# Performance work log

Hardware: AMD Instinct MI355X
Metric: run time of the kernel (lower is better)

## Reference

```python
import jax, jax.numpy as jnp
import numpy as np

B, S, D, H, F = 2, 4096, 768, 12, 3072
DK = D // H
EPS = 1e-5


def _layernorm(x, alpha, gamma):
    # Faithful to the custom Layernormalization: torch.std (unbiased, ddof=1),
    # (x - mean) / (std + eps), scalar alpha/gamma.
    m = jnp.mean(x, axis=-1, keepdims=True)
    s = jnp.std(x, axis=-1, ddof=1, keepdims=True)
    return alpha * ((x - m) / (s + EPS)) + gamma


def setup_inputs() -> dict:
    key = jax.random.key(0)
    ks = jax.random.split(key, 12)
    sc = 0.02
    inp = {
        "x": jax.random.normal(ks[0], (B, S, D), jnp.float32),
        # attention projections, stored as [in, out]
        "wq": jax.random.normal(ks[1], (D, D), jnp.float32) * sc,
        "bq": jnp.zeros((D,), jnp.float32),
        "wk": jax.random.normal(ks[2], (D, D), jnp.float32) * sc,
        "bk": jnp.zeros((D,), jnp.float32),
        "wv": jax.random.normal(ks[3], (D, D), jnp.float32) * sc,
        "bv": jnp.zeros((D,), jnp.float32),
        "wo": jax.random.normal(ks[4], (D, D), jnp.float32) * sc,
        "bo": jnp.zeros((D,), jnp.float32),
        # feedforward
        "w1": jax.random.normal(ks[5], (D, F), jnp.float32) * sc,
        "b1": jnp.zeros((F,), jnp.float32),
        "w2": jax.random.normal(ks[6], (F, D), jnp.float32) * sc,
        "b2": jnp.zeros((D,), jnp.float32),
        # two residual LayerNorms, scalar params (alpha=1, gamma=0 at init)
        "a1": jnp.ones((1,), jnp.float32),
        "g1": jnp.zeros((1,), jnp.float32),
        "a2": jnp.ones((1,), jnp.float32),
        "g2": jnp.zeros((1,), jnp.float32),
    }
    return inp


def reference(x, wq, bq, wk, bk, wv, bv, wo, bo, w1, b1, w2, b2, a1, g1, a2, g2):
    # --- self attention sublayer ---
    q = (x @ wq + bq).reshape(B, S, H, DK).transpose(0, 2, 1, 3)  # [B,H,S,dk]
    k = (x @ wk + bk).reshape(B, S, H, DK).transpose(0, 2, 1, 3)
    v = (x @ wv + bv).reshape(B, S, H, DK).transpose(0, 2, 1, 3)
    scores = jnp.einsum("bhqd,bhkd->bhqk", q, k) / np.sqrt(DK).astype(np.float32)
    attn = jax.nn.softmax(scores, axis=-1)  # dropout is identity (p=0 / eval)
    ctx = jnp.einsum("bhqk,bhkd->bhqd", attn, v)  # [B,H,S,dk]
    ctx = ctx.transpose(0, 2, 1, 3).reshape(B, S, D)
    attn_out = ctx @ wo + bo
    x = _layernorm(x + attn_out, a1, g1)
    # --- feedforward sublayer ---
    ff = jax.nn.relu(x @ w1 + b1) @ w2 + b2
    x = _layernorm(x + ff, a2, g2)
    return x
```

## Files before the change

### kernel.cpp

```cpp
#include <hip/hip_runtime.h>
#include <hip/hip_bf16.h>
#include <cstdint>
#include <cstddef>

typedef unsigned short u16;
typedef __attribute__((ext_vector_type(8))) __bf16 bf16x8;
typedef __attribute__((ext_vector_type(4))) float f32x4;

#define AS1 __attribute__((address_space(1)))
#define AS3 __attribute__((address_space(3)))

__device__ __forceinline__ u16 f2bf(float f) {
    union { float f; uint32_t u; } v; v.f = f;
    uint32_t r = (v.u + 0x7FFFu + ((v.u >> 16) & 1u)) >> 16;
    return (u16)r;
}

__device__ __forceinline__ float bf2f(u16 b) {
    union { uint32_t u; float f; } v; v.u = ((uint32_t)b) << 16;
    return v.f;
}

__device__ __forceinline__ uint32_t pack_bf2(float lo, float hi) {
    __hip_bfloat162 p = __float22bfloat162_rn(float2{lo, hi});
    union { __hip_bfloat162 b; uint32_t u; } v; v.b = p;
    return v.u;
}

__device__ __forceinline__ f32x4 mfma16(bf16x8 a, bf16x8 b, f32x4 c) {
    return __builtin_amdgcn_mfma_f32_16x16x32_bf16(a, b, c, 0, 0, 0);
}

__device__ __forceinline__ void async16(const u16* g, u16* lds_uniform_base) {
    __builtin_amdgcn_global_load_lds((const AS1 void*)g, (AS3 void*)lds_uniform_base, 16, 0, 0);
}

__device__ __forceinline__ int xcd_swz(int nwg) {
    int b = blockIdx.x + gridDim.x * (blockIdx.y + gridDim.y * blockIdx.z);
    return (b & 7) * (nwg >> 3) + (b >> 3);
}

__global__ __launch_bounds__(256)
void k_prep(const float* __restrict__ x, u16* __restrict__ xb,
            const float* __restrict__ wq, const float* __restrict__ wk,
            const float* __restrict__ wv, const float* __restrict__ wo,
            const float* __restrict__ w1, const float* __restrict__ w2,
            u16* __restrict__ wqkvt, u16* __restrict__ wot,
            u16* __restrict__ w1t, u16* __restrict__ w2t)
{
    int bx = blockIdx.x;
    if (bx < 6144) {
        int i = (bx * 256 + threadIdx.x) * 4;
        float4 f = *(const float4*)(x + i);
        xb[i + 0] = f2bf(f.x); xb[i + 1] = f2bf(f.y);
        xb[i + 2] = f2bf(f.z); xb[i + 3] = f2bf(f.w);
        return;
    }
    int t = bx - 6144;
    const float* in; u16* out; int R, C;
    if (t < 2304) {
        int m = t / 576; t -= m * 576;
        R = 768; C = 768;
        in = (m == 0) ? wq : (m == 1) ? wk : (m == 2) ? wv : wo;
        out = (m < 3) ? wqkvt + (size_t)m * 768 * 768 : wot;
    } else if (t < 4608) {
        t -= 2304; in = w1; out = w1t; R = 768; C = 3072;
    } else {
        t -= 4608; in = w2; out = w2t; R = 3072; C = 768;
    }
    int tilesX = C >> 5;
    int c0 = (t % tilesX) * 32, r0 = (t / tilesX) * 32;
    __shared__ float tile[32][33];
    int tx = threadIdx.x & 31, ty = threadIdx.x >> 5;
    #pragma unroll
    for (int i = ty; i < 32; i += 8)
        tile[i][tx] = in[(size_t)(r0 + i) * C + c0 + tx];
    __syncthreads();
    #pragma unroll
    for (int i = ty; i < 32; i += 8)
        out[(size_t)(c0 + i) * R + r0 + tx] = f2bf(tile[tx][i]);
}

template <bool RELU>
__global__ __launch_bounds__(256)
void k_gemm(const u16* __restrict__ A, const u16* __restrict__ Bt,
            const float* __restrict__ bias, u16* __restrict__ Cb,
            int M, int N, int K)
{
    __shared__ __align__(16) u16 lA[2 * 4096];
    __shared__ __align__(16) u16 lB[2 * 4096];
    const int tid = threadIdx.x;
    const int w = tid >> 6, lane = tid & 63;
    const int quad = lane >> 4, l15 = lane & 15;
    const int m0 = blockIdx.x * 128, n0 = blockIdx.y * 128;
    const int wm = (w >> 1) * 64, wn = (w & 1) * 64;
    const int sw = (quad ^ ((l15 >> 1) & 3)) * 8;
    const int dst = (w * 64) * 8;

    const u16* pA[2]; const u16* pB[2];
    #pragma unroll
    for (int r = 0; r < 2; ++r) {
        int c = r * 256 + tid;
        int row = c >> 2, ch = (c & 3) ^ ((row >> 1) & 3);
        pA[r] = A + (size_t)(m0 + row) * K + ch * 8;
        pB[r] = Bt + (size_t)(n0 + row) * K + ch * 8;
    }

    const f32x4 fz = {0.f, 0.f, 0.f, 0.f};
    f32x4 acc[4][4];
    #pragma unroll
    for (int i = 0; i < 4; ++i)
        #pragma unroll
        for (int j = 0; j < 4; ++j) acc[i][j] = fz;

    #pragma unroll
    for (int r = 0; r < 2; ++r) {
        async16(pA[r], lA + r * 2048 + dst);
        async16(pB[r], lB + r * 2048 + dst);
        pA[r] += 32; pB[r] += 32;
    }

    const int nIt = K >> 5;
    for (int it = 0; it < nIt; ++it) {
        __syncthreads();
        if (it + 1 < nIt) {
            int nb = (it + 1) & 1;
            #pragma unroll
            for (int r = 0; r < 2; ++r) {
                async16(pA[r], lA + nb * 4096 + r * 2048 + dst);
                async16(pB[r], lB + nb * 4096 + r * 2048 + dst);
                pA[r] += 32; pB[r] += 32;
            }
        }
        const u16* bA = lA + (it & 1) * 4096;
        const u16* bB = lB + (it & 1) * 4096;
        bf16x8 af[4], bfr[4];
        #pragma unroll
        for (int i = 0; i < 4; ++i)
            af[i] = *(const bf16x8*)&bA[(wm + i * 16 + l15) * 32 + sw];
        #pragma unroll
        for (int j = 0; j < 4; ++j)
            bfr[j] = *(const bf16x8*)&bB[(wn + j * 16 + l15) * 32 + sw];
        #pragma unroll
        for (int i = 0; i < 4; ++i)
            #pragma unroll
            for (int j = 0; j < 4; ++j)
                acc[i][j] = mfma16(af[i], bfr[j], acc[i][j]);
    }
    #pragma unroll
    for (int j = 0; j < 4; ++j) {
        int col = n0 + wn + j * 16 + l15;
        float bv = bias[col];
        #pragma unroll
        for (int i = 0; i < 4; ++i) {
            int row = m0 + wm + i * 16 + quad * 4;
            #pragma unroll
            for (int r = 0; r < 4; ++r) {
                float t = acc[i][j][r] + bv;
                if (RELU) t = fmaxf(t, 0.f);
                Cb[(size_t)(row + r) * N + col] = f2bf(t);
            }
        }
    }
}

__global__ __launch_bounds__(256)
void k_gemm_part(const u16* __restrict__ A, const u16* __restrict__ Bt,
                 float* __restrict__ C0, float* __restrict__ C1,
                 int M, int N, int K, int Kh)
{
    __shared__ __align__(16) u16 lA[2 * 4096];
    __shared__ __align__(16) u16 lB[2 * 4096];
    const int tid = threadIdx.x;
    const int w = tid >> 6, lane = tid & 63;
    const int quad = lane >> 4, l15 = lane & 15;
    const int m0 = blockIdx.x * 128, n0 = blockIdx.y * 128;
    const int wm = (w >> 1) * 64, wn = (w & 1) * 64;
    const int sw = (quad ^ ((l15 >> 1) & 3)) * 8;
    const int kbeg = blockIdx.z * Kh;
    float* __restrict__ C = blockIdx.z ? C1 : C0;
    const int dst = (w * 64) * 8;

    const u16* pA[2]; const u16* pB[2];
    #pragma unroll
    for (int r = 0; r < 2; ++r) {
        int c = r * 256 + tid;
        int row = c >> 2, ch = (c & 3) ^ ((row >> 1) & 3);
        pA[r] = A + (size_t)(m0 + row) * K + kbeg + ch * 8;
        pB[r] = Bt + (size_t)(n0 + row) * K + kbeg + ch * 8;
    }

    const f32x4 fz = {0.f, 0.f, 0.f, 0.f};
    f32x4 acc[4][4];
    #pragma unroll
    for (int i = 0; i < 4; ++i)
        #pragma unroll
        for (int j = 0; j < 4; ++j) acc[i][j] = fz;

    #pragma unroll
    for (int r = 0; r < 2; ++r) {
        async16(pA[r], lA + r * 2048 + dst);
        async16(pB[r], lB + r * 2048 + dst);
        pA[r] += 32; pB[r] += 32;
    }

    const int nIt = Kh >> 5;
    for (int it = 0; it < nIt; ++it) {
        __syncthreads();
        if (it + 1 < nIt) {
            int nb = (it + 1) & 1;
            #pragma unroll
            for (int r = 0; r < 2; ++r) {
                async16(pA[r], lA + nb * 4096 + r * 2048 + dst);
                async16(pB[r], lB + nb * 4096 + r * 2048 + dst);
                pA[r] += 32; pB[r] += 32;
            }
        }
        const u16* bA = lA + (it & 1) * 4096;
        const u16* bB = lB + (it & 1) * 4096;
        bf16x8 af[4], bfr[4];
        #pragma unroll
        for (int i = 0; i < 4; ++i)
            af[i] = *(const bf16x8*)&bA[(wm + i * 16 + l15) * 32 + sw];
        #pragma unroll
        for (int j = 0; j < 4; ++j)
            bfr[j] = *(const bf16x8*)&bB[(wn + j * 16 + l15) * 32 + sw];
        #pragma unroll
        for (int i = 0; i < 4; ++i)
            #pragma unroll
            for (int j = 0; j < 4; ++j)
                acc[i][j] = mfma16(af[i], bfr[j], acc[i][j]);
    }
    #pragma unroll
    for (int j = 0; j < 4; ++j) {
        int col = n0 + wn + j * 16 + l15;
        #pragma unroll
        for (int i = 0; i < 4; ++i) {
            int row = m0 + wm + i * 16 + quad * 4;
            #pragma unroll
            for (int r = 0; r < 4; ++r)
                C[(size_t)(row + r) * N + col] = acc[i][j][r];
        }
    }
}

__global__ __launch_bounds__(256)
void k_gemm_qkv(const u16* __restrict__ A, const u16* __restrict__ Bt,
                const float* __restrict__ bq, const float* __restrict__ bk,
                const float* __restrict__ bv,
                u16* __restrict__ qb, u16* __restrict__ kb, u16* __restrict__ vtg,
                int M, int K, float scale_q)
{
    __shared__ __align__(16) u16 qsm[4 * 64 * 72];
    u16* lA = qsm;
    u16* lB = qsm + 8192;
    const int tid = threadIdx.x;
    const int w = tid >> 6, lane = tid & 63;
    const int quad = lane >> 4, l15 = lane & 15;
    const int m0 = blockIdx.x * 128, n0 = blockIdx.y * 128;
    const int wm = (w >> 1) * 64, wn = (w & 1) * 64;
    const int sw = (quad ^ ((l15 >> 1) & 3)) * 8;
    const int sel = blockIdx.y / 6;
    const int cl0 = n0 - sel * 768;
    const int dst = (w * 64) * 8;

    const u16* pA[2]; const u16* pB[2];
    #pragma unroll
    for (int r = 0; r < 2; ++r) {
        int c = r * 256 + tid;
        int row = c >> 2, ch = (c & 3) ^ ((row >> 1) & 3);
        pA[r] = A + (size_t)(m0 + row) * K + ch * 8;
        pB[r] = Bt + (size_t)(n0 + row) * K + ch * 8;
    }

    const f32x4 fz = {0.f, 0.f, 0.f, 0.f};
    f32x4 acc[4][4];
    #pragma unroll
    for (int i = 0; i < 4; ++i)
        #pragma unroll
        for (int j = 0; j < 4; ++j) acc[i][j] = fz;

    #pragma unroll
    for (int r = 0; r < 2; ++r) {
        async16(pA[r], lA + r * 2048 + dst);
        async16(pB[r], lB + r * 2048 + dst);
        pA[r] += 32; pB[r] += 32;
    }

    const int nIt = K >> 5;
    for (int it = 0; it < nIt; ++it) {
        __syncthreads();
        if (it + 1 < nIt) {
            int nb = (it + 1) & 1;
            #pragma unroll
            for (int r = 0; r < 2; ++r) {
                async16(pA[r], lA + nb * 4096 + r * 2048 + dst);
                async16(pB[r], lB + nb * 4096 + r * 2048 + dst);
                pA[r] += 32; pB[r] += 32;
            }
        }
        const u16* bA = lA + (it & 1) * 4096;
        const u16* bB = lB + (it & 1) * 4096;
        bf16x8 af[4], bfr[4];
        #pragma unroll
        for (int i = 0; i < 4; ++i)
            af[i] = *(const bf16x8*)&bA[(wm + i * 16 + l15) * 32 + sw];
        #pragma unroll
        for (int j = 0; j < 4; ++j)
            bfr[j] = *(const bf16x8*)&bB[(wn + j * 16 + l15) * 32 + sw];
        #pragma unroll
        for (int i = 0; i < 4; ++i)
            #pragma unroll
            for (int j = 0; j < 4; ++j)
                acc[i][j] = mfma16(af[i], bfr[j], acc[i][j]);
    }
    __syncthreads();
    const float* bias = (sel == 0) ? bq : (sel == 1) ? bk : bv;
    if (sel < 2) {
        u16* out = (sel == 0) ? qb : kb;
        float sc = (sel == 0) ? scale_q : 1.f;
        #pragma unroll
        for (int j = 0; j < 4; ++j) {
            int cl = cl0 + wn + j * 16 + l15;
            float bvv = bias[cl];
            #pragma unroll
            for (int i = 0; i < 4; ++i) {
                int row = m0 + wm + i * 16 + quad * 4;
                #pragma unroll
                for (int r = 0; r < 4; ++r)
                    out[(size_t)(row + r) * 768 + cl] = f2bf((acc[i][j][r] + bvv) * sc);
            }
        }
    } else {
        u16* lT = qsm + w * 4608;
        #pragma unroll
        for (int j = 0; j < 4; ++j) {
            float bvv = bias[cl0 + wn + j * 16 + l15];
            #pragma unroll
            for (int i = 0; i < 4; ++i)
                #pragma unroll
                for (int r = 0; r < 4; ++r)
                    lT[(j * 16 + l15) * 72 + i * 16 + quad * 4 + r]
                        = f2bf(acc[i][j][r] + bvv);
        }
        int gcol = cl0 + wn + lane;
        u16* gdst = vtg + (size_t)gcol * M + m0 + wm;
        #pragma unroll
        for (int kk = 0; kk < 8; ++kk) {
            bf16x8 v = *(const bf16x8*)&lT[lane * 72 + kk * 8];
            *(bf16x8*)(gdst + kk * 8) = v;
        }
    }
}

__global__ __launch_bounds__(256, 3)
void k_attention(const u16* __restrict__ Q, const u16* __restrict__ Kb,
                 const u16* __restrict__ Vt, u16* __restrict__ ctx,
                 int S, int D, int H, int M)
{
    __shared__ __align__(16) u16 sKV[16384];
    __shared__ float sL[2][64];
    const int o = xcd_swz(gridDim.x * gridDim.y);
    const int qt = o % gridDim.x, bh = o / gridDim.x;
    const int b = bh / H, h = bh % H;
    const int tid = threadIdx.x, w = tid >> 6, lane = tid & 63;
    const int wq = w & 1, wk = w >> 1;
    const int quad = lane >> 4, l15 = lane & 15;
    const int sw = (quad ^ ((l15 >> 1) & 3)) * 8;
    const size_t bS = (size_t)b * S;
    const int q0 = qt * 128 + wq * 64;

    bf16x8 qf[4][2];
    #pragma unroll
    for (int set = 0; set < 4; ++set)
        #pragma unroll
        for (int kc = 0; kc < 2; ++kc)
            qf[set][kc] = *(const bf16x8*)(Q + (bS + q0 + set * 16 + l15) * D
                                           + (size_t)h * 64 + kc * 32 + quad * 8);

    const f32x4 fz = {0.f, 0.f, 0.f, 0.f};
    f32x4 O[4][4], Ol[4];
    #pragma unroll
    for (int s = 0; s < 4; ++s) {
        Ol[s] = fz;
        #pragma unroll
        for (int j = 0; j < 4; ++j) O[s][j] = fz;
    }
    union { u16 s[8]; bf16x8 v; } one8;
    #pragma unroll
    for (int i = 0; i < 8; ++i) one8.s[i] = 0x3F80;

    const u16* kbase = Kb + bS * D + (size_t)h * 64;
    const u16* vbase = Vt + (size_t)h * 64 * M + bS;

    const int rsw = (lane & ~12) | ((lane & 4) << 1) | ((lane & 8) >> 1);
    const u16* gk[2]; const u16* gv[2];
    #pragma unroll
    for (int i = 0; i < 2; ++i) {
        gk[i] = kbase + (size_t)rsw * D + i * 32 + w * 8;
        int c = i * 256 + tid;
        int dk = (c >> 2) & 63, vch = (c & 3) ^ ((dk >> 1) & 3);
        gv[i] = vbase + (size_t)dk * M + i * 32 + vch * 8;
    }
    const int dslot = w * 512;

    #pragma unroll
    for (int i = 0; i < 2; ++i) {
        async16(gk[i], sKV + i * 2048 + dslot);
        async16(gv[i], sKV + 8192 + i * 2048 + dslot);
        gk[i] += (size_t)64 * D;
        gv[i] += 64;
    }

    int ksl[2];
    #pragma unroll
    for (int ks = 0; ks < 2; ++ks) {
        int row64 = wk * 32 + ((l15 >> 2) << 3) + ks * 4 + (l15 & 3);
        int s = (row64 & ~12) | ((row64 & 4) << 1) | ((row64 & 8) >> 1);
        ksl[ks] = quad * 512 + s * 8;
    }

    const int T = S >> 6;
    for (int t = 0; t < T; ++t) {
        __syncthreads();
        if (t + 1 < T) {
            int nb = (t + 1) & 1;
            #pragma unroll
            for (int i = 0; i < 2; ++i) {
                async16(gk[i], sKV + nb * 4096 + i * 2048 + dslot);
                async16(gv[i], sKV + 8192 + nb * 4096 + i * 2048 + dslot);
                gk[i] += (size_t)64 * D;
                gv[i] += 64;
            }
        }
        const u16* lKb = sKV + (t & 1) * 4096;
        const u16* lVb = sKV + 8192 + (t & 1) * 4096;

        bf16x8 ka[2][2], vf[4];
        #pragma unroll
        for (int ks = 0; ks < 2; ++ks)
            #pragma unroll
            for (int kc = 0; kc < 2; ++kc)
                ka[ks][kc] = *(const bf16x8*)&lKb[kc * 2048 + ksl[ks]];
        #pragma unroll
        for (int dj = 0; dj < 4; ++dj)
            vf[dj] = *(const bf16x8*)
                &lVb[wk * 2048 + (dj * 16 + l15) * 32 + sw];

        #pragma unroll
        for (int set = 0; set < 4; ++set) {
            f32x4 sc0 = fz, sc1 = fz;
            __builtin_amdgcn_s_setprio(1);
            sc0 = mfma16(ka[0][0], qf[set][0], sc0);
            sc0 = mfma16(ka[0][1], qf[set][1], sc0);
            sc1 = mfma16(ka[1][0], qf[set][0], sc1);
            sc1 = mfma16(ka[1][1], qf[set][1], sc1);
            __builtin_amdgcn_s_setprio(0);
            float p0[4], p1[4];
            #pragma unroll
            for (int r = 0; r < 4; ++r) {
                p0[r] = __builtin_amdgcn_exp2f(sc0[r]);
                p1[r] = __builtin_amdgcn_exp2f(sc1[r]);
            }
            union { uint32_t u[4]; bf16x8 v; } pa;
            pa.u[0] = pack_bf2(p0[0], p0[1]); pa.u[1] = pack_bf2(p0[2], p0[3]);
            pa.u[2] = pack_bf2(p1[0], p1[1]); pa.u[3] = pack_bf2(p1[2], p1[3]);
            __builtin_amdgcn_s_setprio(1);
            #pragma unroll
            for (int dj = 0; dj < 4; ++dj)
                O[set][dj] = mfma16(pa.v, vf[dj], O[set][dj]);
            Ol[set] = mfma16(pa.v, one8.v, Ol[set]);
            __builtin_amdgcn_s_setprio(0);
        }
    }

    __syncthreads();
    u16* lO = sKV;
    if (wk == 1) {
        #pragma unroll
        for (int set = 0; set < 4; ++set) {
            #pragma unroll
            for (int dj = 0; dj < 4; ++dj)
                #pragma unroll
                for (int r = 0; r < 4; ++r)
                    lO[(wq * 64 + set * 16 + quad * 4 + r) * 66 + dj * 16 + l15]
                        = f2bf(O[set][dj][r]);
            if (l15 == 0) {
                #pragma unroll
                for (int r = 0; r < 4; ++r)
                    sL[wq][set * 16 + quad * 4 + r] = Ol[set][r];
            }
        }
    }
    __syncthreads();
    if (wk == 0) {
        #pragma unroll
        for (int set = 0; set < 4; ++set) {
            float rl[4];
            #pragma unroll
            for (int r = 0; r < 4; ++r)
                rl[r] = 1.f / (Ol[set][r] + sL[wq][set * 16 + quad * 4 + r]);
            #pragma unroll
            for (int dj = 0; dj < 4; ++dj)
                #pragma unroll
                for (int r = 0; r < 4; ++r) {
                    float o = O[set][dj][r]
                        + bf2f(lO[(wq * 64 + set * 16 + quad * 4 + r) * 66 + dj * 16 + l15]);
                    ctx[(bS + q0 + set * 16 + quad * 4 + r) * D
                        + (size_t)h * 64 + dj * 16 + l15] = f2bf(o * rl[r]);
                }
        }
    }
}

__global__ __launch_bounds__(256)
void k_layernorm2(const float* __restrict__ p0, const float* __restrict__ p1,
                  const float* __restrict__ resid, const float* __restrict__ bias,
                  const float* __restrict__ a, const float* __restrict__ g,
                  float* __restrict__ outf, u16* __restrict__ outb, int D)
{
    const int row = blockIdx.x, tid = threadIdx.x;
    const size_t base = (size_t)row * D;
    float v[3];
    float s = 0.f, sq = 0.f;
    #pragma unroll
    for (int i = 0; i < 3; ++i) {
        int c = tid + i * 256;
        float x = p0[base + c] + p1[base + c] + resid[base + c] + bias[c];
        v[i] = x; s += x; sq += x * x;
    }
    #pragma unroll
    for (int off = 32; off >= 1; off >>= 1) {
        s += __shfl_xor(s, off, 64);
        sq += __shfl_xor(sq, off, 64);
    }
    __shared__ float red[8];
    const int w = tid >> 6;
    if ((tid & 63) == 0) { red[w] = s; red[4 + w] = sq; }
    __syncthreads();
    s = red[0] + red[1] + red[2] + red[3];
    sq = red[4] + red[5] + red[6] + red[7];
    float mean = s / D;
    float var = fmaxf((sq - s * mean) / (D - 1), 0.f);
    float denom = sqrtf(var) + 1e-5f;
    float av = a[0], gv = g[0];
    #pragma unroll
    for (int i = 0; i < 3; ++i) {
        float y = av * ((v[i] - mean) / denom) + gv;
        if (outf) outf[base + tid + i * 256] = y;
        if (outb) outb[base + tid + i * 256] = f2bf(y);
    }
}

extern "C" void kernel_launch(void* const* d_in, const int* in_sizes, int n_in,
                              void* d_out, int out_size, void* d_ws, size_t ws_size,
                              hipStream_t stream)
{
    constexpr int B = 2, S = 4096, D = 768, H = 12, F = 3072;
    constexpr int M = B * S;
    const float SCALE_Q = 1.4426950408889634f / 8.0f;
    const float* x  = (const float*)d_in[0];
    const float* wq = (const float*)d_in[1];
    const float* bq = (const float*)d_in[2];
    const float* wk = (const float*)d_in[3];
    const float* bk = (const float*)d_in[4];
    const float* wv = (const float*)d_in[5];
    const float* bv = (const float*)d_in[6];
    const float* wo = (const float*)d_in[7];
    const float* bo = (const float*)d_in[8];
    const float* w1 = (const float*)d_in[9];
    const float* b1 = (const float*)d_in[10];
    const float* w2 = (const float*)d_in[11];
    const float* b2 = (const float*)d_in[12];
    const float* a1 = (const float*)d_in[13];
    const float* g1 = (const float*)d_in[14];
    const float* a2 = (const float*)d_in[15];
    const float* g2 = (const float*)d_in[16];

    char* ws = (char*)d_ws;
    size_t off = 0;
    auto alloc = [&](size_t bytes) {
        void* p = ws + off;
        off = (off + bytes + 255) & ~(size_t)255;
        return p;
    };
    u16*   xb    = (u16*)alloc((size_t)M * D * 2);
    u16*   wqkvt = (u16*)alloc((size_t)3 * D * D * 2);
    u16*   wot   = (u16*)alloc((size_t)D * D * 2);
    u16*   w1t   = (u16*)alloc((size_t)D * F * 2);
    u16*   w2t   = (u16*)alloc((size_t)D * F * 2);
    u16*   qb    = (u16*)alloc((size_t)M * D * 2);
    u16*   kb    = (u16*)alloc((size_t)M * D * 2);
    u16*   vtg   = (u16*)alloc((size_t)M * D * 2);
    u16*   ctxb  = (u16*)alloc((size_t)M * D * 2);
    float* x1f   = (float*)alloc((size_t)M * D * 4);
    u16*   x1b   = (u16*)alloc((size_t)M * D * 2);
    u16*   ff1b  = (u16*)alloc((size_t)M * F * 2);

    float* p0a = (float*)qb;
    float* p1a = (float*)ff1b;
    float* p0b = (float*)qb;
    float* p1b = (float*)vtg;

    k_prep<<<6144 + 6912, 256, 0, stream>>>(x, xb, wq, wk, wv, wo, w1, w2,
                                            wqkvt, wot, w1t, w2t);

    k_gemm_qkv<<<dim3(M / 128, 3 * D / 128), 256, 0, stream>>>(
        xb, wqkvt, bq, bk, bv, qb, kb, vtg, M, D, SCALE_Q);

    k_attention<<<dim3(S / 128, B * H), 256, 0, stream>>>(qb, kb, vtg, ctxb, S, D, H, M);

    k_gemm_part<<<dim3(M / 128, D / 128, 2), 256, 0, stream>>>(
        ctxb, wot, p0a, p1a, M, D, D, D / 2);
    k_layernorm2<<<M, 256, 0, stream>>>(p0a, p1a, x, bo, a1, g1, x1f, x1b, D);

    k_gemm<true><<<dim3(M / 128, F / 128), 256, 0, stream>>>(
        x1b, w1t, b1, ff1b, M, F, D);
    k_gemm_part<<<dim3(M / 128, D / 128, 2), 256, 0, stream>>>(
        ff1b, w2t, p0b, p1b, M, D, F, F / 2);
    k_layernorm2<<<M, 256, 0, stream>>>(p0b, p1b, x1f, b2, a2, g2, (float*)d_out, nullptr, D);

    (void)in_sizes; (void)n_in; (void)out_size; (void)ws_size;
}
```

Baseline: 451.7 us.

## Triple-buffer GEMM LDS tiles with prefetch distance two and explicit vmcnt waits

Converts the three GEMM kernels (generic, split-K partial, QKV) from double-buffered to triple-buffered LDS staging. Two K-tiles are issued ahead and each iteration waits only for the oldest group via s_waitcnt vmcnt(4) before a raw s_barrier, instead of a full __syncthreads drain. The goal is to keep more global loads in flight so memory latency hides behind the MFMA work. In exchange LDS use per block grows from 32 KB to 48 KB, which may lower occupancy, and correctness now depends on the exact count of outstanding async loads per thread.

```diff
diff --git a/kernel.cpp b/kernel.cpp
--- a/kernel.cpp
+++ b/kernel.cpp
@@ -87,15 +87,15 @@
             const float* __restrict__ bias, u16* __restrict__ Cb,
             int M, int N, int K)
 {
-    __shared__ __align__(16) u16 lA[2 * 4096];
-    __shared__ __align__(16) u16 lB[2 * 4096];
+    __shared__ __align__(16) u16 lA[3 * 4096];
+    __shared__ __align__(16) u16 lB[3 * 4096];
     const int tid = threadIdx.x;
     const int w = tid >> 6, lane = tid & 63;
     const int quad = lane >> 4, l15 = lane & 15;
     const int m0 = blockIdx.x * 128, n0 = blockIdx.y * 128;
     const int wm = (w >> 1) * 64, wn = (w & 1) * 64;
     const int sw = (quad ^ ((l15 >> 1) & 3)) * 8;
-    const int dst = (w * 64) * 8;
+    const int dst = w * 512;
 
     const u16* pA[2]; const u16* pB[2];
     #pragma unroll
@@ -114,17 +114,24 @@
         for (int j = 0; j < 4; ++j) acc[i][j] = fz;
 
     #pragma unroll
-    for (int r = 0; r < 2; ++r) {
-        async16(pA[r], lA + r * 2048 + dst);
-        async16(pB[r], lB + r * 2048 + dst);
-        pA[r] += 32; pB[r] += 32;
+    for (int p = 0; p < 2; ++p) {
+        #pragma unroll
+        for (int r = 0; r < 2; ++r) {
+            async16(pA[r], lA + p * 4096 + r * 2048 + dst);
+            async16(pB[r], lB + p * 4096 + r * 2048 + dst);
+            pA[r] += 32; pB[r] += 32;
+        }
     }
 
     const int nIt = K >> 5;
+    int cur = 0;
     for (int it = 0; it < nIt; ++it) {
-        __syncthreads();
-        if (it + 1 < nIt) {
-            int nb = (it + 1) & 1;
+        if (it + 1 < nIt) asm volatile("s_waitcnt vmcnt(4)" ::: "memory");
+        else              asm volatile("s_waitcnt vmcnt(0)" ::: "memory");
+        __builtin_amdgcn_s_barrier();
+        asm volatile("" ::: "memory");
+        if (it + 2 < nIt) {
+            int nb = cur + 2; if (nb >= 3) nb -= 3;
             #pragma unroll
             for (int r = 0; r < 2; ++r) {
                 async16(pA[r], lA + nb * 4096 + r * 2048 + dst);
@@ -132,8 +139,8 @@
                 pA[r] += 32; pB[r] += 32;
             }
         }
-        const u16* bA = lA + (it & 1) * 4096;
-        const u16* bB = lB + (it & 1) * 4096;
+        const u16* bA = lA + cur * 4096;
+        const u16* bB = lB + cur * 4096;
         bf16x8 af[4], bfr[4];
         #pragma unroll
         for (int i = 0; i < 4; ++i)
@@ -146,6 +153,8 @@
             #pragma unroll
             for (int j = 0; j < 4; ++j)
                 acc[i][j] = mfma16(af[i], bfr[j], acc[i][j]);
+        asm volatile("" ::: "memory");
+        cur = (cur + 1 == 3) ? 0 : cur + 1;
     }
     #pragma unroll
     for (int j = 0; j < 4; ++j) {
@@ -169,8 +178,8 @@
                  float* __restrict__ C0, float* __restrict__ C1,
                  int M, int N, int K, int Kh)
 {
-    __shared__ __align__(16) u16 lA[2 * 4096];
-    __shared__ __align__(16) u16 lB[2 * 4096];
+    __shared__ __align__(16) u16 lA[3 * 4096];
+    __shared__ __align__(16) u16 lB[3 * 4096];
     const int tid = threadIdx.x;
     const int w = tid >> 6, lane = tid & 63;
     const int quad = lane >> 4, l15 = lane & 15;
@@ -179,7 +188,7 @@
     const int sw = (quad ^ ((l15 >> 1) & 3)) * 8;
     const int kbeg = blockIdx.z * Kh;
     float* __restrict__ C = blockIdx.z ? C1 : C0;
-    const int dst = (w * 64) * 8;
+    const int dst = w * 512;
 
     const u16* pA[2]; const u16* pB[2];
     #pragma unroll
@@ -198,17 +207,24 @@
         for (int j = 0; j < 4; ++j) acc[i][j] = fz;
 
     #pragma unroll
-    for (int r = 0; r < 2; ++r) {
-        async16(pA[r], lA + r * 2048 + dst);
-        async16(pB[r], lB + r * 2048 + dst);
-        pA[r] += 32; pB[r] += 32;
+    for (int p = 0; p < 2; ++p) {
+        #pragma unroll
+        for (int r = 0; r < 2; ++r) {
+            async16(pA[r], lA + p * 4096 + r * 2048 + dst);
+            async16(pB[r], lB + p * 4096 + r * 2048 + dst);
+            pA[r] += 32; pB[r] += 32;
+        }
     }
 
     const int nIt = Kh >> 5;
+    int cur = 0;
     for (int it = 0; it < nIt; ++it) {
-        __syncthreads();
-        if (it + 1 < nIt) {
-            int nb = (it + 1) & 1;
+        if (it + 1 < nIt) asm volatile("s_waitcnt vmcnt(4)" ::: "memory");
+        else              asm volatile("s_waitcnt vmcnt(0)" ::: "memory");
+        __builtin_amdgcn_s_barrier();
+        asm volatile("" ::: "memory");
+        if (it + 2 < nIt) {
+            int nb = cur + 2; if (nb >= 3) nb -= 3;
             #pragma unroll
             for (int r = 0; r < 2; ++r) {
                 async16(pA[r], lA + nb * 4096 + r * 2048 + dst);
@@ -216,8 +232,8 @@
                 pA[r] += 32; pB[r] += 32;
             }
         }
-        const u16* bA = lA + (it & 1) * 4096;
-        const u16* bB = lB + (it & 1) * 4096;
+        const u16* bA = lA + cur * 4096;
+        const u16* bB = lB + cur * 4096;
         bf16x8 af[4], bfr[4];
         #pragma unroll
         for (int i = 0; i < 4; ++i)
@@ -230,6 +246,8 @@
             #pragma unroll
             for (int j = 0; j < 4; ++j)
                 acc[i][j] = mfma16(af[i], bfr[j], acc[i][j]);
+        asm volatile("" ::: "memory");
+        cur = (cur + 1 == 3) ? 0 : cur + 1;
     }
     #pragma unroll
     for (int j = 0; j < 4; ++j) {
@@ -251,9 +269,9 @@
                 u16* __restrict__ qb, u16* __restrict__ kb, u16* __restrict__ vtg,
                 int M, int K, float scale_q)
 {
-    __shared__ __align__(16) u16 qsm[4 * 64 * 72];
+    __shared__ __align__(16) u16 qsm[24576];
     u16* lA = qsm;
-    u16* lB = qsm + 8192;
+    u16* lB = qsm + 12288;
     const int tid = threadIdx.x;
     const int w = tid >> 6, lane = tid & 63;
     const int quad = lane >> 4, l15 = lane & 15;
@@ -262,7 +280,7 @@
     const int sw = (quad ^ ((l15 >> 1) & 3)) * 8;
     const int sel = blockIdx.y / 6;
     const int cl0 = n0 - sel * 768;
-    const int dst = (w * 64) * 8;
+    const int dst = w * 512;
 
     const u16* pA[2]; const u16* pB[2];
     #pragma unroll
@@ -281,17 +299,24 @@
         for (int j = 0; j < 4; ++j) acc[i][j] = fz;
 
     #pragma unroll
-    for (int r = 0; r < 2; ++r) {
-        async16(pA[r], lA + r * 2048 + dst);
-        async16(pB[r], lB + r * 2048 + dst);
-        pA[r] += 32; pB[r] += 32;
+    for (int p = 0; p < 2; ++p) {
+        #pragma unroll
+        for (int r = 0; r < 2; ++r) {
+            async16(pA[r], lA + p * 4096 + r * 2048 + dst);
+            async16(pB[r], lB + p * 4096 + r * 2048 + dst);
+            pA[r] += 32; pB[r] += 32;
+        }
     }
 
     const int nIt = K >> 5;
+    int cur = 0;
     for (int it = 0; it < nIt; ++it) {
-        __syncthreads();
-        if (it + 1 < nIt) {
-            int nb = (it + 1) & 1;
+        if (it + 1 < nIt) asm volatile("s_waitcnt vmcnt(4)" ::: "memory");
+        else              asm volatile("s_waitcnt vmcnt(0)" ::: "memory");
+        __builtin_amdgcn_s_barrier();
+        asm volatile("" ::: "memory");
+        if (it + 2 < nIt) {
+            int nb = cur + 2; if (nb >= 3) nb -= 3;
             #pragma unroll
             for (int r = 0; r < 2; ++r) {
                 async16(pA[r], lA + nb * 4096 + r * 2048 + dst);
@@ -299,8 +324,8 @@
                 pA[r] += 32; pB[r] += 32;
             }
         }
-        const u16* bA = lA + (it & 1) * 4096;
-        const u16* bB = lB + (it & 1) * 4096;
+        const u16* bA = lA + cur * 4096;
+        const u16* bB = lB + cur * 4096;
         bf16x8 af[4], bfr[4];
         #pragma unroll
         for (int i = 0; i < 4; ++i)
@@ -313,6 +338,8 @@
             #pragma unroll
             for (int j = 0; j < 4; ++j)
                 acc[i][j] = mfma16(af[i], bfr[j], acc[i][j]);
+        asm volatile("" ::: "memory");
+        cur = (cur + 1 == 3) ? 0 : cur + 1;
     }
     __syncthreads();
     const float* bias = (sel == 0) ? bq : (sel == 1) ? bk : bv;
```

Result: no change. 449.6 us (-0.5%).
